# Kernel optimization log

Measured on AMD Instinct MI355X. Metric: run time of the kernel, lower is better.

Reference implementation:

```python
import jax, jax.numpy as jnp
import numpy as np


def setup_inputs() -> dict:
    key = jax.random.key(0)
    B, N, M, D = 8, 256, 16, 256
    embeddings = jax.random.normal(key, (B, N, M, D), dtype=jnp.float32)
    w = jnp.asarray(10.0, dtype=jnp.float32)
    b = jnp.asarray(-5.0, dtype=jnp.float32)
    return {"embeddings": embeddings, "w": w, "b": b}


def reference(embeddings, w, b):
    # embeddings: [B, N, M, D]
    B, N, M, D = embeddings.shape
    centroids = jnp.mean(embeddings, axis=2)  # [B, N, D]

    # Cross similarities: S[b,j,i,k] = w * <e_{bji}, c_{bk}> + b
    S = w * jnp.einsum('bjid,bkd->bjik', embeddings, centroids) + b  # [B,N,M,N]

    # Own-centroid case (j == k): leave-one-out centroid
    # <e, (M*c_j - e)/(M-1)> = (M*<e,c_j> - ||e||^2) / (M-1)
    dot_own = jnp.einsum('bjid,bjd->bji', embeddings, centroids)     # [B,N,M]
    sq_norm = jnp.sum(embeddings * embeddings, axis=-1)              # [B,N,M]
    S_self = w * (M * dot_own - sq_norm) / (M - 1) + b               # [B,N,M]

    # Place S_self on the k == j diagonal
    eye = jnp.eye(N, dtype=bool)[None, :, None, :]                   # [1,N,1,N]
    S = jnp.where(eye, S_self[..., None], S)

    # loss = sum log sum_k exp(S) - sum_{j==k} S
    loss = jnp.sum(jax.nn.logsumexp(S, axis=-1)) - jnp.sum(S_self)
    return loss
```

## Files before the change

kernel.cpp:

```cpp
#include <hip/hip_runtime.h>

constexpr int B = 8, N = 256, M = 16, D = 256;

typedef short bf16x8 __attribute__((ext_vector_type(8)));
typedef float f32x4 __attribute__((ext_vector_type(4)));

__device__ __forceinline__ unsigned short f2bf(float x) {
  unsigned u = __float_as_uint(x);
  u = (u + 0x7FFFu + ((u >> 16) & 1u)) >> 16;
  return (unsigned short)u;
}
__device__ __forceinline__ uint4 packbf8(const float* f) {
  uint4 u;
  u.x = (unsigned)f2bf(f[0]) | ((unsigned)f2bf(f[1]) << 16);
  u.y = (unsigned)f2bf(f[2]) | ((unsigned)f2bf(f[3]) << 16);
  u.z = (unsigned)f2bf(f[4]) | ((unsigned)f2bf(f[5]) << 16);
  u.w = (unsigned)f2bf(f[6]) | ((unsigned)f2bf(f[7]) << 16);
  return u;
}


__global__ __launch_bounds__(256) void k_prep(const float* __restrict__ e,
                                              uint4* __restrict__ Cbf,
                                              float* __restrict__ out) {
  const int blk = blockIdx.x;
  const int b = blk >> 8, j = blk & 255;
  const int t = threadIdx.x;
  const float* base = e + (size_t)blk * (M * D);
  float s = 0.f;
#pragma unroll
  for (int i = 0; i < M; ++i) s += base[i * D + t];
  __shared__ float cl[D];
  cl[t] = s * (1.f / 16.f);
  __syncthreads();
  if (t < 32) {
    const int kc = t >> 2, qq = t & 3;
    float f[8];
#pragma unroll
    for (int x = 0; x < 8; ++x) f[x] = cl[kc * 32 + qq * 8 + x];
    Cbf[(size_t)((b * 8 + kc) * 16 + (j >> 4)) * 64 + qq * 16 + (j & 15)] = packbf8(f);
  }
  if (blk == 0 && t == 0) out[0] = 0.f;
}

__global__ __launch_bounds__(256) void k_gemm(const float* __restrict__ e,
                                              const uint4* __restrict__ Cbf,
                                              const float* __restrict__ wp,
                                              const float* __restrict__ bp,
                                              float* __restrict__ out) {
  const int blk = blockIdx.x;
  const int b = blk >> 6, strip = blk & 63;
  const int tid = threadIdx.x;
  const int wid = tid >> 6, lane = tid & 63;
  const int h = wid >> 1, c = wid & 1;
  const int q = lane >> 4, m = lane & 15;

  const float* Abase =
      e + (size_t)b * (N * M * D) + (size_t)((strip * 4 + h * 2) * 16 + m) * D + q * 8;
  const uint4* Bb = Cbf + (size_t)(b * 128 + c * 8) * 64 + lane;

  f32x4 acc[2][8];
#pragma unroll
  for (int rt = 0; rt < 2; ++rt)
#pragma unroll
    for (int nt = 0; nt < 8; ++nt) acc[rt][nt] = (f32x4)0.f;
  float sqp[2] = {0.f, 0.f};

#pragma unroll 1
  for (int kc = 0; kc < 8; ++kc) {
    float fa[2][8];
#pragma unroll
    for (int rt = 0; rt < 2; ++rt) {
      const float4 lo = *(const float4*)(Abase + (size_t)rt * 16 * D + kc * 32);
      const float4 hi = *(const float4*)(Abase + (size_t)rt * 16 * D + kc * 32 + 4);
      fa[rt][0] = lo.x; fa[rt][1] = lo.y; fa[rt][2] = lo.z; fa[rt][3] = lo.w;
      fa[rt][4] = hi.x; fa[rt][5] = hi.y; fa[rt][6] = hi.z; fa[rt][7] = hi.w;
#pragma unroll
      for (int x = 0; x < 8; ++x) sqp[rt] = fmaf(fa[rt][x], fa[rt][x], sqp[rt]);
    }
    uint4 a0 = packbf8(fa[0]);
    uint4 a1 = packbf8(fa[1]);
    uint4 bfr[8];
#pragma unroll
    for (int nt = 0; nt < 8; ++nt) bfr[nt] = Bb[(kc * 16 + nt) * 64];
    bf16x8 av0 = __builtin_bit_cast(bf16x8, a0);
    bf16x8 av1 = __builtin_bit_cast(bf16x8, a1);
#pragma unroll
    for (int nt = 0; nt < 8; ++nt) {
      bf16x8 bv = __builtin_bit_cast(bf16x8, bfr[nt]);
      acc[0][nt] = __builtin_amdgcn_mfma_f32_16x16x32_bf16(av0, bv, acc[0][nt], 0, 0, 0);
      acc[1][nt] = __builtin_amdgcn_mfma_f32_16x16x32_bf16(av1, bv, acc[1][nt], 0, 0, 0);
    }
  }

#pragma unroll
  for (int rt = 0; rt < 2; ++rt) {
    sqp[rt] += __shfl_xor(sqp[rt], 16, 64);
    sqp[rt] += __shfl_xor(sqp[rt], 32, 64);
  }
  float sqv[2][4];
#pragma unroll
  for (int rt = 0; rt < 2; ++rt)
#pragma unroll
    for (int reg = 0; reg < 4; ++reg) sqv[rt][reg] = __shfl(sqp[rt], q * 4 + reg, 64);

  const float w = *wp, bias = *bp;
  __shared__ float lmx[2][64];
  __shared__ float lsm[2][64];
  __shared__ float bred[4];
  float ssum = 0.f;

#pragma unroll
  for (int rt = 0; rt < 2; ++rt) {
    const int jr = strip * 4 + h * 2 + rt;
    const bool own = (c == (jr >> 7)) && (m == (jr & 15));
    const int ntd = (jr >> 4) & 7;
#pragma unroll
    for (int nt = 0; nt < 8; ++nt)
#pragma unroll
      for (int reg = 0; reg < 4; ++reg) {
        const float raw = acc[rt][nt][reg];
        float sv = fmaf(w, raw, bias);
        if (own && nt == ntd) {
          sv = fmaf(w * (1.f / 15.f), 16.f * raw - sqv[rt][reg], bias);
          ssum += sv;
        }
        acc[rt][nt][reg] = sv;
      }
#pragma unroll
    for (int reg = 0; reg < 4; ++reg) {
      float mx = acc[rt][0][reg];
#pragma unroll
      for (int nt = 1; nt < 8; ++nt) mx = fmaxf(mx, acc[rt][nt][reg]);
#pragma unroll
      for (int mk = 1; mk < 16; mk <<= 1) mx = fmaxf(mx, __shfl_xor(mx, mk, 64));
      if (m == 0) lmx[c][(h * 2 + rt) * 16 + q * 4 + reg] = mx;
    }
  }
  __syncthreads();

#pragma unroll
  for (int rt = 0; rt < 2; ++rt)
#pragma unroll
    for (int reg = 0; reg < 4; ++reg) {
      const int Rl = (h * 2 + rt) * 16 + q * 4 + reg;
      const float mx = fmaxf(lmx[0][Rl], lmx[1][Rl]);
      float se = 0.f;
#pragma unroll
      for (int nt = 0; nt < 8; ++nt) se += __expf(acc[rt][nt][reg] - mx);
#pragma unroll
      for (int mk = 1; mk < 16; mk <<= 1) se += __shfl_xor(se, mk, 64);
      if (m == 0) lsm[c][Rl] = se;
    }
  __syncthreads();

  float part = -ssum;
  if (c == 0 && m == 0) {
#pragma unroll
    for (int rt = 0; rt < 2; ++rt)
#pragma unroll
      for (int reg = 0; reg < 4; ++reg) {
        const int Rl = (h * 2 + rt) * 16 + q * 4 + reg;
        const float mx = fmaxf(lmx[0][Rl], lmx[1][Rl]);
        part += mx + __logf(lsm[0][Rl] + lsm[1][Rl]);
      }
  }
#pragma unroll
  for (int mk = 1; mk < 64; mk <<= 1) part += __shfl_xor(part, mk, 64);
  if (lane == 0) bred[wid] = part;
  __syncthreads();
  if (tid == 0) atomicAdd(out, bred[0] + bred[1] + bred[2] + bred[3]);
}

extern "C" void kernel_launch(void* const* d_in, const int* in_sizes, int n_in,
                              void* d_out, int out_size, void* d_ws, size_t ws_size,
                              hipStream_t stream) {
  const float* e = (const float*)d_in[0];
  const float* wp = (const float*)d_in[1];
  const float* bp = (const float*)d_in[2];
  float* out = (float*)d_out;
  uint4* Cbf = (uint4*)d_ws;

  k_prep<<<B * N, 256, 0, stream>>>(e, Cbf, out);
  k_gemm<<<B * 64, 256, 0, stream>>>(e, Cbf, wp, bp, out);
}
```

Baseline: 98.66 us.

## Fuse centroid prep and GEMM into one cooperative kernel with grid sync

Replaces the two-kernel sequence with a single cooperative kernel of 256 blocks. Each block loads its rows of embeddings once, computes the centroids by wave shuffles, keeps the bf16-packed A operand in registers across a grid-wide barrier, then runs the MFMA GEMM and logsumexp. This removes the second full read of the 32MB input and one kernel launch. In exchange it adds a grid sync, higher register pressure from 4 row tiles per wave, and only 256 blocks at one block per CU. The old two-kernel path is kept as a fallback if the cooperative launch fails.

```diff
diff --git a/kernel.cpp b/kernel.cpp
--- a/kernel.cpp
+++ b/kernel.cpp
@@ -1,4 +1,7 @@
 #include <hip/hip_runtime.h>
+#include <hip/hip_cooperative_groups.h>
+
+namespace cg = cooperative_groups;
 
 constexpr int B = 8, N = 256, M = 16, D = 256;
 
@@ -19,6 +22,160 @@
   return u;
 }
 
+
+__global__ __launch_bounds__(256, 1) void k_fused(const float* __restrict__ e,
+                                                  uint4* __restrict__ Cbf,
+                                                  const float* __restrict__ wp,
+                                                  const float* __restrict__ bp,
+                                                  float* __restrict__ out) {
+  const int blk = blockIdx.x;
+  const int b = blk >> 5, sp = blk & 31;
+  const int tid = threadIdx.x;
+  const int wid = tid >> 6, lane = tid & 63;
+  const int h = wid >> 1, c = wid & 1;
+  const int q = lane >> 4, m = lane & 15;
+
+  if (blk == 0 && tid == 0) out[0] = 0.f;
+
+  uint4 a_bf[4][8];
+  float sqp[4];
+#pragma unroll
+  for (int t4 = 0; t4 < 4; ++t4) {
+    const int st = t4 >> 1, rt = t4 & 1;
+    const int lt = st * 4 + h * 2 + rt;
+    const int jr = sp * 8 + lt;
+    const float* rbase = e + ((size_t)(b * N + jr) * M + m) * D + q * 8;
+    float sq = 0.f;
+#pragma unroll
+    for (int kc = 0; kc < 8; ++kc) {
+      const float4 lo = *(const float4*)(rbase + kc * 32);
+      const float4 hi = *(const float4*)(rbase + kc * 32 + 4);
+      float f[8] = {lo.x, lo.y, lo.z, lo.w, hi.x, hi.y, hi.z, hi.w};
+#pragma unroll
+      for (int x = 0; x < 8; ++x) sq = fmaf(f[x], f[x], sq);
+      a_bf[t4][kc] = packbf8(f);
+      float cv[8];
+#pragma unroll
+      for (int x = 0; x < 8; ++x) cv[x] = f[x];
+#pragma unroll
+      for (int mk = 1; mk < 16; mk <<= 1)
+#pragma unroll
+        for (int x = 0; x < 8; ++x) cv[x] += __shfl_xor(cv[x], mk, 64);
+      if (m == (jr & 15)) {
+        float cs[8];
+#pragma unroll
+        for (int x = 0; x < 8; ++x) cs[x] = cv[x] * (1.f / 16.f);
+        Cbf[((size_t)(b * 8 + kc) * 16 + (jr >> 4)) * 64 + q * 16 + (jr & 15)] =
+            packbf8(cs);
+      }
+    }
+    sq += __shfl_xor(sq, 16, 64);
+    sq += __shfl_xor(sq, 32, 64);
+    sqp[t4] = sq;
+  }
+  float sqv[4][4];
+#pragma unroll
+  for (int t4 = 0; t4 < 4; ++t4)
+#pragma unroll
+    for (int reg = 0; reg < 4; ++reg) sqv[t4][reg] = __shfl(sqp[t4], q * 4 + reg, 64);
+
+  __threadfence();
+  cg::this_grid().sync();
+
+  const uint4* Bb = Cbf + (size_t)(b * 128 + c * 8) * 64 + lane;
+  f32x4 acc[4][8];
+#pragma unroll
+  for (int t4 = 0; t4 < 4; ++t4)
+#pragma unroll
+    for (int nt = 0; nt < 8; ++nt) acc[t4][nt] = (f32x4)0.f;
+
+#pragma unroll
+  for (int kc = 0; kc < 8; ++kc) {
+    uint4 bfr[8];
+#pragma unroll
+    for (int nt = 0; nt < 8; ++nt) bfr[nt] = Bb[(kc * 16 + nt) * 64];
+#pragma unroll
+    for (int nt = 0; nt < 8; ++nt) {
+      const bf16x8 bv = __builtin_bit_cast(bf16x8, bfr[nt]);
+#pragma unroll
+      for (int t4 = 0; t4 < 4; ++t4)
+        acc[t4][nt] = __builtin_amdgcn_mfma_f32_16x16x32_bf16(
+            __builtin_bit_cast(bf16x8, a_bf[t4][kc]), bv, acc[t4][nt], 0, 0, 0);
+    }
+  }
+
+  const float w = *wp, bias = *bp;
+  __shared__ float lmx[2][128];
+  __shared__ float lsm[2][128];
+  __shared__ float bred[4];
+  float ssum = 0.f;
+
+#pragma unroll
+  for (int t4 = 0; t4 < 4; ++t4) {
+    const int lt = (t4 >> 1) * 4 + h * 2 + (t4 & 1);
+    const int jr = sp * 8 + lt;
+    const bool own = (c == (jr >> 7)) && (m == (jr & 15));
+    const int ntd = (jr >> 4) & 7;
+#pragma unroll
+    for (int nt = 0; nt < 8; ++nt)
+#pragma unroll
+      for (int reg = 0; reg < 4; ++reg) {
+        const float raw = acc[t4][nt][reg];
+        float sv = fmaf(w, raw, bias);
+        if (own && nt == ntd) {
+          sv = fmaf(w * (1.f / 15.f), 16.f * raw - sqv[t4][reg], bias);
+          ssum += sv;
+        }
+        acc[t4][nt][reg] = sv;
+      }
+#pragma unroll
+    for (int reg = 0; reg < 4; ++reg) {
+      float mx = acc[t4][0][reg];
+#pragma unroll
+      for (int nt = 1; nt < 8; ++nt) mx = fmaxf(mx, acc[t4][nt][reg]);
+#pragma unroll
+      for (int mk = 1; mk < 16; mk <<= 1) mx = fmaxf(mx, __shfl_xor(mx, mk, 64));
+      if (m == 0) lmx[c][lt * 16 + q * 4 + reg] = mx;
+    }
+  }
+  __syncthreads();
+
+#pragma unroll
+  for (int t4 = 0; t4 < 4; ++t4) {
+    const int lt = (t4 >> 1) * 4 + h * 2 + (t4 & 1);
+#pragma unroll
+    for (int reg = 0; reg < 4; ++reg) {
+      const int Rl = lt * 16 + q * 4 + reg;
+      const float mx = fmaxf(lmx[0][Rl], lmx[1][Rl]);
+      float se = 0.f;
+#pragma unroll
+      for (int nt = 0; nt < 8; ++nt) se += __expf(acc[t4][nt][reg] - mx);
+#pragma unroll
+      for (int mk = 1; mk < 16; mk <<= 1) se += __shfl_xor(se, mk, 64);
+      if (m == 0) lsm[c][Rl] = se;
+    }
+  }
+  __syncthreads();
+
+  float part = -ssum;
+  if (c == 0 && m == 0) {
+#pragma unroll
+    for (int t4 = 0; t4 < 4; ++t4) {
+      const int lt = (t4 >> 1) * 4 + h * 2 + (t4 & 1);
+#pragma unroll
+      for (int reg = 0; reg < 4; ++reg) {
+        const int Rl = lt * 16 + q * 4 + reg;
+        const float mx = fmaxf(lmx[0][Rl], lmx[1][Rl]);
+        part += mx + __logf(lsm[0][Rl] + lsm[1][Rl]);
+      }
+    }
+  }
+#pragma unroll
+  for (int mk = 1; mk < 64; mk <<= 1) part += __shfl_xor(part, mk, 64);
+  if (lane == 0) bred[wid] = part;
+  __syncthreads();
+  if (tid == 0) atomicAdd(out, bred[0] + bred[1] + bred[2] + bred[3]);
+}
 
 __global__ __launch_bounds__(256) void k_prep(const float* __restrict__ e,
                                               uint4* __restrict__ Cbf,
@@ -181,6 +338,11 @@
   float* out = (float*)d_out;
   uint4* Cbf = (uint4*)d_ws;
 
-  k_prep<<<B * N, 256, 0, stream>>>(e, Cbf, out);
-  k_gemm<<<B * 64, 256, 0, stream>>>(e, Cbf, wp, bp, out);
-}
+  void* args[] = {(void*)&e, (void*)&Cbf, (void*)&wp, (void*)&bp, (void*)&out};
+  hipError_t rc = hipLaunchCooperativeKernel((const void*)k_fused, dim3(B * 32),
+                                             dim3(256), args, 0, stream);
+  if (rc != hipSuccess) {
+    k_prep<<<B * N, 256, 0, stream>>>(e, Cbf, out);
+    k_gemm<<<B * 64, 256, 0, stream>>>(e, Cbf, wp, bp, out);
+  }
+}
```

Measured after the change: 185.5 us. 1.88x slower.
